# Kernel tuning notes

Measured on AMD Instinct MI355X. Metric: run time of the kernel, lower is better.

## Reference

```python
import math
import jax, jax.numpy as jnp
import numpy as np

HEADS = 8


def setup_inputs() -> dict:
    key = jax.random.key(0)
    k1, k2 = jax.random.split(key)
    b, heads, c, t, s_enc = 4, HEADS, 64, 1024, 1024
    x = jax.random.normal(k1, (b, 3 * heads * c, t), dtype=jnp.float32)
    encoder_kv = jax.random.normal(k2, (b, 2 * heads * c, s_enc), dtype=jnp.float32)
    return {"x": x, "encoder_kv": encoder_kv}


def reference(x, encoder_kv):
    heads = HEADS
    b, ch3, t = x.shape
    c = ch3 // (3 * heads)
    s_enc = encoder_kv.shape[-1]
    # 'b (qkv heads c) h -> qkv (b heads) c h'
    qkv = x.reshape(b, 3, heads, c, t).transpose(1, 0, 2, 3, 4).reshape(3, b * heads, c, t)
    q, k, v = qkv[0], qkv[1], qkv[2]
    ekv = encoder_kv.reshape(b, 2, heads, c, s_enc).transpose(1, 0, 2, 3, 4).reshape(2, b * heads, c, s_enc)
    ek, ev = ekv[0], ekv[1]
    k = jnp.concatenate([ek, k], axis=-1)  # (bh, c, s_enc + t)
    v = jnp.concatenate([ev, v], axis=-1)
    scale = 1.0 / math.sqrt(math.sqrt(c))
    weight = jnp.einsum('bct,bcs->bts', q * scale, k * scale)  # (bh, t, s)
    weight = jax.nn.softmax(weight.astype(jnp.float32), axis=-1).astype(weight.dtype)
    out = jnp.einsum('bts,bcs->bct', weight, v)  # (bh, c, t)
    # '(b heads) c h -> b (heads c) h'
    out = out.reshape(b, heads, c, t).reshape(b, heads * c, t)
    return out
```

## Files before the change

kernel.cpp:

```cpp
#include <hip/hip_runtime.h>

typedef __attribute__((ext_vector_type(8))) short bf16x8;
typedef __attribute__((ext_vector_type(4))) float f32x4;

#define BQ 64
#define SK 64
#define LDS_P 72
#define NH 8
#define CD 64
#define TLEN 1024
#define SENC 1024
#define STOT 2048
#define NIT (STOT / SK)

#define QSCALE 0.18033688f
#define M2     12.98425550f

__device__ __forceinline__ ushort f2bf(float f) {
  uint x = __builtin_bit_cast(uint, f);
  uint r = (x + 0x7fffu + ((x >> 16) & 1u)) >> 16;
  return (ushort)r;
}
__device__ __forceinline__ uint4 pack8(const ushort* p) {
  uint4 u;
  u.x = (uint)p[0] | ((uint)p[1] << 16);
  u.y = (uint)p[2] | ((uint)p[3] << 16);
  u.z = (uint)p[4] | ((uint)p[5] << 16);
  u.w = (uint)p[6] | ((uint)p[7] << 16);
  return u;
}

__global__ __launch_bounds__(256)
void repack_kernel(const float* __restrict__ x, const float* __restrict__ ekv,
                   ushort* __restrict__ ktw, ushort* __restrict__ vnw) {
  const int kx = blockIdx.x;
  const int bh = blockIdx.y;
  const int b = bh >> 3, h = bh & 7;
  const int t = threadIdx.x;
  const float* ks;
  const float* vs;
  if (kx < 16) {
    ks = ekv + (size_t)(b * 2 * NH * CD + h * CD) * SENC + kx * 64;
    vs = ekv + (size_t)(b * 2 * NH * CD + NH * CD + h * CD) * SENC + kx * 64;
  } else {
    ks = x + (size_t)(b * 3 * NH * CD + NH * CD + h * CD) * TLEN + (kx - 16) * 64;
    vs = x + (size_t)(b * 3 * NH * CD + 2 * NH * CD + h * CD) * TLEN + (kx - 16) * 64;
  }
  if (blockIdx.z == 0) {
    __shared__ float Lt[64 * 65];
    const int ci = t >> 2, seg = t & 3;
#pragma unroll
    for (int j = 0; j < 4; ++j) {
      float4 d = *(const float4*)&ks[ci * 1024 + seg * 16 + 4 * j];
      Lt[ci * 65 + seg * 16 + 4 * j + 0] = d.x;
      Lt[ci * 65 + seg * 16 + 4 * j + 1] = d.y;
      Lt[ci * 65 + seg * 16 + 4 * j + 2] = d.z;
      Lt[ci * 65 + seg * 16 + 4 * j + 3] = d.w;
    }
    __syncthreads();
    const int key = t >> 2;
    ushort tmp[16];
#pragma unroll
    for (int u = 0; u < 16; ++u)
      tmp[u] = f2bf(Lt[(seg * 16 + u) * 65 + key]);
    ushort* dst = ktw + ((size_t)bh * STOT + kx * 64 + key) * CD + seg * 16;
    *(uint4*)dst = pack8(tmp);
    *(uint4*)(dst + 8) = pack8(tmp + 8);
  } else {
    const int ci = t >> 2, seg = t & 3;
    ushort tmp[16];
#pragma unroll
    for (int j = 0; j < 4; ++j) {
      float4 d = *(const float4*)&vs[ci * 1024 + seg * 16 + 4 * j];
      tmp[4 * j + 0] = f2bf(d.x);
      tmp[4 * j + 1] = f2bf(d.y);
      tmp[4 * j + 2] = f2bf(d.z);
      tmp[4 * j + 3] = f2bf(d.w);
    }
    ushort* dst = vnw + (size_t)bh * CD * STOT + (size_t)ci * STOT + kx * 64 + seg * 16;
    *(uint4*)dst = pack8(tmp);
    *(uint4*)(dst + 8) = pack8(tmp + 8);
  }
}

__global__ __launch_bounds__(256, 3)
void qkv_attn_ws(const float* __restrict__ x, const ushort* __restrict__ ktw,
                 const ushort* __restrict__ vnw, float* __restrict__ out) {
  __shared__ __align__(16) ushort Kb[2][SK * LDS_P];
  __shared__ __align__(16) ushort Vb[2][CD * LDS_P];
  __shared__ __align__(16) ushort Pw[4 * 16 * LDS_P];

  const int tid  = threadIdx.x;
  const int w    = tid >> 6;
  const int lane = tid & 63;
  const int quad = lane >> 4;
  const int l16  = lane & 15;

  const int f  = blockIdx.x;
  const int bh = (f & 7) + 8 * (f >> 7);
  const int qt = (f >> 3) & 15;
  const int b  = bh >> 3;
  const int h  = bh & 7;
  const int t0 = qt * BQ;

  const float* qg = x + (size_t)(b * 3 * NH * CD + h * CD) * TLEN;
  float* og = out + (size_t)(b * NH * CD + h * CD) * TLEN;
  const ushort* ktb = ktw + (size_t)bh * STOT * CD;
  const ushort* vnb = vnw + (size_t)bh * CD * STOT;

#pragma unroll
  for (int e = 0; e < 16; ++e) {
    int ci = 4 * e + w;
    Kb[1][lane * LDS_P + ci] = f2bf(qg[ci * TLEN + t0 + lane] * QSCALE);
  }
  __syncthreads();
  bf16x8 qfrag[2];
#pragma unroll
  for (int kst = 0; kst < 2; ++kst)
    qfrag[kst] = *(const bf16x8*)&Kb[1][(w * 16 + l16) * LDS_P + kst * 32 + quad * 8];

  const int row = tid >> 2, seg = tid & 3;
  uint4 kp0 = *(const uint4*)(ktb + (size_t)row * CD + seg * 16);
  uint4 kp1 = *(const uint4*)(ktb + (size_t)row * CD + seg * 16 + 8);
  uint4 vp0 = *(const uint4*)(vnb + (size_t)row * STOT + seg * 16);
  uint4 vp1 = *(const uint4*)(vnb + (size_t)row * STOT + seg * 16 + 8);
  *(uint4*)&Kb[0][row * LDS_P + seg * 16]     = kp0;
  *(uint4*)&Kb[0][row * LDS_P + seg * 16 + 8] = kp1;
  *(uint4*)&Vb[0][row * LDS_P + seg * 16]     = vp0;
  *(uint4*)&Vb[0][row * LDS_P + seg * 16 + 8] = vp1;
  __syncthreads();

  f32x4 ofrag[4];
#pragma unroll
  for (int mt = 0; mt < 4; ++mt) ofrag[mt] = f32x4{0.f, 0.f, 0.f, 0.f};
  float l_acc = 0.f;

  for (int it = 0; it < NIT; ++it) {
    const int cur = it & 1;

    if (it + 1 < NIT) {
      const int s1 = (it + 1) * SK;
      kp0 = *(const uint4*)(ktb + ((size_t)(s1 + row)) * CD + seg * 16);
      kp1 = *(const uint4*)(ktb + ((size_t)(s1 + row)) * CD + seg * 16 + 8);
      vp0 = *(const uint4*)(vnb + (size_t)row * STOT + s1 + seg * 16);
      vp1 = *(const uint4*)(vnb + (size_t)row * STOT + s1 + seg * 16 + 8);
    }

    float ps[4][4];
#pragma unroll
    for (int mt = 0; mt < 4; ++mt) {
      f32x4 acc = f32x4{0.f, 0.f, 0.f, 0.f};
#pragma unroll
      for (int kst = 0; kst < 2; ++kst) {
        bf16x8 afr = *(const bf16x8*)&Kb[cur][(mt * 16 + l16) * LDS_P + kst * 32 + quad * 8];
        acc = __builtin_amdgcn_mfma_f32_16x16x32_bf16(afr, qfrag[kst], acc, 0, 0, 0);
      }
#pragma unroll
      for (int r = 0; r < 4; ++r) ps[mt][r] = acc[r];
    }

    ushort* pws = &Pw[w * 16 * LDS_P];
#pragma unroll
    for (int mt = 0; mt < 4; ++mt) {
      float p0 = exp2f(ps[mt][0] - M2);
      float p1 = exp2f(ps[mt][1] - M2);
      float p2 = exp2f(ps[mt][2] - M2);
      float p3 = exp2f(ps[mt][3] - M2);
      l_acc += (p0 + p1) + (p2 + p3);
      uint lo = (uint)f2bf(p0) | ((uint)f2bf(p1) << 16);
      uint hi = (uint)f2bf(p2) | ((uint)f2bf(p3) << 16);
      *(uint2*)&pws[l16 * LDS_P + mt * 16 + quad * 4] = make_uint2(lo, hi);
    }
    __asm__ __volatile__("s_waitcnt lgkmcnt(0)" ::: "memory");

    bf16x8 pfr[2];
#pragma unroll
    for (int kst = 0; kst < 2; ++kst)
      pfr[kst] = *(const bf16x8*)&Pw[(w * 16 + l16) * LDS_P + kst * 32 + quad * 8];
#pragma unroll
    for (int mt = 0; mt < 4; ++mt) {
#pragma unroll
      for (int kst = 0; kst < 2; ++kst) {
        bf16x8 vfr = *(const bf16x8*)&Vb[cur][(mt * 16 + l16) * LDS_P + kst * 32 + quad * 8];
        ofrag[mt] = __builtin_amdgcn_mfma_f32_16x16x32_bf16(vfr, pfr[kst], ofrag[mt], 0, 0, 0);
      }
    }

    if (it + 1 < NIT) {
      *(uint4*)&Kb[1 - cur][row * LDS_P + seg * 16]     = kp0;
      *(uint4*)&Kb[1 - cur][row * LDS_P + seg * 16 + 8] = kp1;
      *(uint4*)&Vb[1 - cur][row * LDS_P + seg * 16]     = vp0;
      *(uint4*)&Vb[1 - cur][row * LDS_P + seg * 16 + 8] = vp1;
      __syncthreads();
    }
  }

  {
    float lv = l_acc;
    lv += __shfl_xor(lv, 16);
    lv += __shfl_xor(lv, 32);
    float inv = 1.0f / lv;
#pragma unroll
    for (int mt = 0; mt < 4; ++mt) {
#pragma unroll
      for (int r = 0; r < 4; ++r) {
        int ci = mt * 16 + quad * 4 + r;
        og[ci * TLEN + t0 + w * 16 + l16] = ofrag[mt][r] * inv;
      }
    }
  }
}

extern "C" void kernel_launch(void* const* d_in, const int* in_sizes, int n_in,
                              void* d_out, int out_size, void* d_ws, size_t ws_size,
                              hipStream_t stream) {
  const float* x   = (const float*)d_in[0];
  const float* ekv = (const float*)d_in[1];
  float* out = (float*)d_out;
  ushort* ktw = (ushort*)d_ws;
  ushort* vnw = ktw + (size_t)32 * STOT * CD;
  repack_kernel<<<dim3(32, 32, 2), 256, 0, stream>>>(x, ekv, ktw, vnw);
  qkv_attn_ws<<<512, 256, 0, stream>>>(x, ktw, vnw, out);
}
```

Before: 128.3 us.

## Split attention over key ranges with atomic accumulation and 32x32 MFMA

Adds a split-K attention kernel in which each block handles one of four 512-key slices for 128 queries. Each wave works on 32 queries using 32x32x16 bf16 MFMA, reading K and V fragments straight from global memory with no LDS staging or block barriers. Partial outputs and row sums are combined with float atomicAdd into a zeroed output buffer, and a finalize kernel then divides by the row sums. The aim is to double the grid to 1024 blocks for better occupancy and to use larger MFMA tiles. The cost is two memsets, atomic traffic on the output, an extra pass over it, and a workspace-size check that falls back to the old kernel.

```diff
diff --git a/kernel.cpp b/kernel.cpp
--- a/kernel.cpp
+++ b/kernel.cpp
@@ -2,16 +2,15 @@
 
 typedef __attribute__((ext_vector_type(8))) short bf16x8;
 typedef __attribute__((ext_vector_type(4))) float f32x4;
-
-#define BQ 64
-#define SK 64
-#define LDS_P 72
+typedef __attribute__((ext_vector_type(16))) float f32x16;
+
 #define NH 8
 #define CD 64
 #define TLEN 1024
 #define SENC 1024
 #define STOT 2048
-#define NIT (STOT / SK)
+#define SK 64
+#define LDS_P 72
 
 #define QSCALE 0.18033688f
 #define M2     12.98425550f
@@ -20,6 +19,9 @@
   uint x = __builtin_bit_cast(uint, f);
   uint r = (x + 0x7fffu + ((x >> 16) & 1u)) >> 16;
   return (ushort)r;
+}
+__device__ __forceinline__ uint pkbf(float a, float b) {
+  return (uint)f2bf(a) | ((uint)f2bf(b) << 16);
 }
 __device__ __forceinline__ uint4 pack8(const ushort* p) {
   uint4 u;
@@ -84,30 +86,151 @@
 }
 
 __global__ __launch_bounds__(256, 3)
+void qkv_attn_split(const float* __restrict__ x, const ushort* __restrict__ ktw,
+                    const ushort* __restrict__ vnw, float* __restrict__ out,
+                    float* __restrict__ pl) {
+  __shared__ __align__(16) ushort Pw[4][32 * LDS_P];
+
+  const int tid  = threadIdx.x;
+  const int w    = tid >> 6;
+  const int lane = tid & 63;
+  const int hi   = lane >> 5;
+  const int l32  = lane & 31;
+
+  const int f   = blockIdx.x;
+  const int bh  = (f & 7) + 8 * (f >> 8);
+  const int mid = (f >> 3) & 31;
+  const int qg  = mid >> 2;
+  const int sp  = mid & 3;
+  const int b = bh >> 3, h = bh & 7;
+  const int q0  = qg * 128 + w * 32;
+  const int s0b = sp * 512;
+
+  const float* qgp = x + (size_t)(b * 3 * NH * CD + h * CD) * TLEN;
+  const ushort* ktb = ktw + (size_t)bh * STOT * CD;
+  const ushort* vnb = vnw + (size_t)bh * CD * STOT;
+  float* og = out + (size_t)(b * NH * CD + h * CD) * TLEN;
+
+  bf16x8 qf[4];
+#pragma unroll
+  for (int kt = 0; kt < 4; ++kt) {
+    uint u0, u1, u2, u3;
+    {
+      const float* qc = qgp + (size_t)(kt * 16 + hi * 8) * TLEN + q0 + l32;
+      float a0 = qc[0 * TLEN] * QSCALE, a1 = qc[1 * TLEN] * QSCALE;
+      float a2 = qc[2 * TLEN] * QSCALE, a3 = qc[3 * TLEN] * QSCALE;
+      float a4 = qc[4 * TLEN] * QSCALE, a5 = qc[5 * TLEN] * QSCALE;
+      float a6 = qc[6 * TLEN] * QSCALE, a7 = qc[7 * TLEN] * QSCALE;
+      u0 = pkbf(a0, a1); u1 = pkbf(a2, a3); u2 = pkbf(a4, a5); u3 = pkbf(a6, a7);
+    }
+    qf[kt] = __builtin_bit_cast(bf16x8, make_uint4(u0, u1, u2, u3));
+  }
+
+  f32x16 oa0 = {0,0,0,0,0,0,0,0,0,0,0,0,0,0,0,0};
+  f32x16 oa1 = {0,0,0,0,0,0,0,0,0,0,0,0,0,0,0,0};
+  float l_acc = 0.f;
+  ushort* pws = &Pw[w][l32 * LDS_P];
+
+  for (int it = 0; it < 8; ++it) {
+    const int s0 = s0b + it * SK;
+
+    bf16x8 kf[2][4];
+    const ushort* kr = ktb + (size_t)(s0 + l32) * CD + hi * 8;
+#pragma unroll
+    for (int mt = 0; mt < 2; ++mt)
+#pragma unroll
+      for (int kt = 0; kt < 4; ++kt)
+        kf[mt][kt] = *(const bf16x8*)(kr + (size_t)mt * 32 * CD + kt * 16);
+
+    f32x16 st0 = {0,0,0,0,0,0,0,0,0,0,0,0,0,0,0,0};
+    f32x16 st1 = {0,0,0,0,0,0,0,0,0,0,0,0,0,0,0,0};
+#pragma unroll
+    for (int kt = 0; kt < 4; ++kt) {
+      st0 = __builtin_amdgcn_mfma_f32_32x32x16_bf16(kf[0][kt], qf[kt], st0, 0, 0, 0);
+      st1 = __builtin_amdgcn_mfma_f32_32x32x16_bf16(kf[1][kt], qf[kt], st1, 0, 0, 0);
+    }
+
+    bf16x8 vf[2][4];
+    const ushort* vr = vnb + (size_t)l32 * STOT + s0 + hi * 8;
+#pragma unroll
+    for (int mt2 = 0; mt2 < 2; ++mt2)
+#pragma unroll
+      for (int kt2 = 0; kt2 < 4; ++kt2)
+        vf[mt2][kt2] = *(const bf16x8*)(vr + (size_t)mt2 * 32 * STOT + kt2 * 16);
+
+#pragma unroll
+    for (int mt = 0; mt < 2; ++mt) {
+      const f32x16 st = mt ? st1 : st0;
+      float p[16];
+#pragma unroll
+      for (int r = 0; r < 16; ++r) {
+        p[r] = exp2f(st[r] - M2);
+        l_acc += p[r];
+      }
+#pragma unroll
+      for (int g = 0; g < 4; ++g) {
+        uint lo = pkbf(p[4 * g + 0], p[4 * g + 1]);
+        uint hh = pkbf(p[4 * g + 2], p[4 * g + 3]);
+        *(uint2*)&pws[mt * 32 + 8 * g + 4 * hi] = make_uint2(lo, hh);
+      }
+    }
+    __asm__ __volatile__("s_waitcnt lgkmcnt(0)" ::: "memory");
+
+    bf16x8 pf[4];
+#pragma unroll
+    for (int kt2 = 0; kt2 < 4; ++kt2)
+      pf[kt2] = *(const bf16x8*)&pws[kt2 * 16 + hi * 8];
+
+#pragma unroll
+    for (int kt2 = 0; kt2 < 4; ++kt2) {
+      oa0 = __builtin_amdgcn_mfma_f32_32x32x16_bf16(vf[0][kt2], pf[kt2], oa0, 0, 0, 0);
+      oa1 = __builtin_amdgcn_mfma_f32_32x32x16_bf16(vf[1][kt2], pf[kt2], oa1, 0, 0, 0);
+    }
+  }
+
+  l_acc += __shfl_xor(l_acc, 32);
+  if (hi == 0) atomicAdd(&pl[bh * TLEN + q0 + l32], l_acc);
+#pragma unroll
+  for (int mt2 = 0; mt2 < 2; ++mt2) {
+    const f32x16 oa = mt2 ? oa1 : oa0;
+#pragma unroll
+    for (int r = 0; r < 16; ++r) {
+      int ci = mt2 * 32 + (r & 3) + 8 * (r >> 2) + 4 * hi;
+      atomicAdd(&og[(size_t)ci * TLEN + q0 + l32], oa[r]);
+    }
+  }
+}
+
+__global__ __launch_bounds__(256)
+void finalize_kernel(float* __restrict__ out, const float* __restrict__ pl) {
+  int i = blockIdx.x * 256 + threadIdx.x;
+  float4 v = ((const float4*)out)[i];
+  int flat = i * 4;
+  int bh = flat >> 16;
+  int t  = flat & 1023;
+  const float4 lv = *(const float4*)&pl[bh * 1024 + t];
+  v.x /= lv.x; v.y /= lv.y; v.z /= lv.z; v.w /= lv.w;
+  ((float4*)out)[i] = v;
+}
+
+#define BQ 64
+#define NIT (STOT / SK)
+__global__ __launch_bounds__(256, 3)
 void qkv_attn_ws(const float* __restrict__ x, const ushort* __restrict__ ktw,
                  const ushort* __restrict__ vnw, float* __restrict__ out) {
   __shared__ __align__(16) ushort Kb[2][SK * LDS_P];
   __shared__ __align__(16) ushort Vb[2][CD * LDS_P];
   __shared__ __align__(16) ushort Pw[4 * 16 * LDS_P];
-
-  const int tid  = threadIdx.x;
-  const int w    = tid >> 6;
-  const int lane = tid & 63;
-  const int quad = lane >> 4;
-  const int l16  = lane & 15;
-
-  const int f  = blockIdx.x;
+  const int tid = threadIdx.x, w = tid >> 6, lane = tid & 63;
+  const int quad = lane >> 4, l16 = lane & 15;
+  const int f = blockIdx.x;
   const int bh = (f & 7) + 8 * (f >> 7);
   const int qt = (f >> 3) & 15;
-  const int b  = bh >> 3;
-  const int h  = bh & 7;
-  const int t0 = qt * BQ;
-
+  const int b = bh >> 3, h = bh & 7, t0 = qt * BQ;
   const float* qg = x + (size_t)(b * 3 * NH * CD + h * CD) * TLEN;
   float* og = out + (size_t)(b * NH * CD + h * CD) * TLEN;
   const ushort* ktb = ktw + (size_t)bh * STOT * CD;
   const ushort* vnb = vnw + (size_t)bh * CD * STOT;
-
 #pragma unroll
   for (int e = 0; e < 16; ++e) {
     int ci = 4 * e + w;
@@ -118,7 +241,6 @@
 #pragma unroll
   for (int kst = 0; kst < 2; ++kst)
     qfrag[kst] = *(const bf16x8*)&Kb[1][(w * 16 + l16) * LDS_P + kst * 32 + quad * 8];
-
   const int row = tid >> 2, seg = tid & 3;
   uint4 kp0 = *(const uint4*)(ktb + (size_t)row * CD + seg * 16);
   uint4 kp1 = *(const uint4*)(ktb + (size_t)row * CD + seg * 16 + 8);
@@ -129,15 +251,12 @@
   *(uint4*)&Vb[0][row * LDS_P + seg * 16]     = vp0;
   *(uint4*)&Vb[0][row * LDS_P + seg * 16 + 8] = vp1;
   __syncthreads();
-
   f32x4 ofrag[4];
 #pragma unroll
   for (int mt = 0; mt < 4; ++mt) ofrag[mt] = f32x4{0.f, 0.f, 0.f, 0.f};
   float l_acc = 0.f;
-
   for (int it = 0; it < NIT; ++it) {
     const int cur = it & 1;
-
     if (it + 1 < NIT) {
       const int s1 = (it + 1) * SK;
       kp0 = *(const uint4*)(ktb + ((size_t)(s1 + row)) * CD + seg * 16);
@@ -145,7 +264,6 @@
       vp0 = *(const uint4*)(vnb + (size_t)row * STOT + s1 + seg * 16);
       vp1 = *(const uint4*)(vnb + (size_t)row * STOT + s1 + seg * 16 + 8);
     }
-
     float ps[4][4];
 #pragma unroll
     for (int mt = 0; mt < 4; ++mt) {
@@ -158,7 +276,6 @@
 #pragma unroll
       for (int r = 0; r < 4; ++r) ps[mt][r] = acc[r];
     }
-
     ushort* pws = &Pw[w * 16 * LDS_P];
 #pragma unroll
     for (int mt = 0; mt < 4; ++mt) {
@@ -167,12 +284,10 @@
       float p2 = exp2f(ps[mt][2] - M2);
       float p3 = exp2f(ps[mt][3] - M2);
       l_acc += (p0 + p1) + (p2 + p3);
-      uint lo = (uint)f2bf(p0) | ((uint)f2bf(p1) << 16);
-      uint hi = (uint)f2bf(p2) | ((uint)f2bf(p3) << 16);
-      *(uint2*)&pws[l16 * LDS_P + mt * 16 + quad * 4] = make_uint2(lo, hi);
+      *(uint2*)&pws[l16 * LDS_P + mt * 16 + quad * 4] =
+          make_uint2(pkbf(p0, p1), pkbf(p2, p3));
     }
     __asm__ __volatile__("s_waitcnt lgkmcnt(0)" ::: "memory");
-
     bf16x8 pfr[2];
 #pragma unroll
     for (int kst = 0; kst < 2; ++kst)
@@ -185,7 +300,6 @@
         ofrag[mt] = __builtin_amdgcn_mfma_f32_16x16x32_bf16(vfr, pfr[kst], ofrag[mt], 0, 0, 0);
       }
     }
-
     if (it + 1 < NIT) {
       *(uint4*)&Kb[1 - cur][row * LDS_P + seg * 16]     = kp0;
       *(uint4*)&Kb[1 - cur][row * LDS_P + seg * 16 + 8] = kp1;
@@ -194,7 +308,6 @@
       __syncthreads();
     }
   }
-
   {
     float lv = l_acc;
     lv += __shfl_xor(lv, 16);
@@ -219,6 +332,15 @@
   float* out = (float*)d_out;
   ushort* ktw = (ushort*)d_ws;
   ushort* vnw = ktw + (size_t)32 * STOT * CD;
+  float*  pl  = (float*)(vnw + (size_t)32 * STOT * CD);
+  const size_t need_split = (size_t)32 * STOT * CD * 2 * 2 + (size_t)32 * TLEN * 4;
   repack_kernel<<<dim3(32, 32, 2), 256, 0, stream>>>(x, ekv, ktw, vnw);
-  qkv_attn_ws<<<512, 256, 0, stream>>>(x, ktw, vnw, out);
-}
+  if (ws_size >= need_split) {
+    hipMemsetAsync(out, 0, (size_t)out_size * 4, stream);
+    hipMemsetAsync(pl, 0, (size_t)32 * TLEN * 4, stream);
+    qkv_attn_split<<<1024, 256, 0, stream>>>(x, ktw, vnw, out, pl);
+    finalize_kernel<<<2048, 256, 0, stream>>>(out, pl);
+  } else {
+    qkv_attn_ws<<<512, 256, 0, stream>>>(x, ktw, vnw, out);
+  }
+}
```

After: 166.4 us. +29.7%, slower.
